# Kernel optimization log

Hardware: AMD Instinct MI355X
Metric: run time of the kernel (lower is better)

## Reference

```python
import jax, jax.numpy as jnp
import numpy as np

B, NIMG, H, W, C = 4, 4, 80, 80, 256
NH = 8
C1 = C // 8          # 32
CPH = C1 // NH       # 4 per-head conv channels
K2D = 4              # deformable attention sampling points
HD2 = C1 // NH       # 4 head dim for 2D deformable attention
INNER = 32           # 3D deformable attention inner dim
DSF = (2, 8, 8)
OSC = jnp.array([2.0, 8.0, 8.0], jnp.float32)


def _bilin2d(img, px, py):
    # img [B,C,H,W]; px,py [B,K] pixel coords -> [B,K,C], zero-padded outside
    Bb, Cc, Hh, Ww = img.shape
    x0 = jnp.floor(px); y0 = jnp.floor(py)
    wx = px - x0; wy = py - y0
    bidx = jnp.arange(Bb)[:, None]
    def g(yy, xx):
        valid = (xx >= 0) & (xx <= Ww - 1) & (yy >= 0) & (yy <= Hh - 1)
        xi = jnp.clip(xx, 0, Ww - 1).astype(jnp.int32)
        yi = jnp.clip(yy, 0, Hh - 1).astype(jnp.int32)
        return img[bidx, :, yi, xi] * valid[..., None]
    return (g(y0, x0) * ((1 - wy) * (1 - wx))[..., None]
          + g(y0, x0 + 1) * ((1 - wy) * wx)[..., None]
          + g(y0 + 1, x0) * (wy * (1 - wx))[..., None]
          + g(y0 + 1, x0 + 1) * (wy * wx)[..., None])


def _trilin(img, z, y, x):
    # img [B,C,D,H,W]; z,y,x [B,K] -> [B,K,C]
    Bb, Cc, Dd, Hh, Ww = img.shape
    z0 = jnp.floor(z); y0 = jnp.floor(y); x0 = jnp.floor(x)
    wz = z - z0; wy = y - y0; wx = x - x0
    bidx = jnp.arange(Bb)[:, None]
    def g(zz, yy, xx):
        valid = (zz >= 0) & (zz <= Dd - 1) & (yy >= 0) & (yy <= Hh - 1) & (xx >= 0) & (xx <= Ww - 1)
        zi = jnp.clip(zz, 0, Dd - 1).astype(jnp.int32)
        yi = jnp.clip(yy, 0, Hh - 1).astype(jnp.int32)
        xi = jnp.clip(xx, 0, Ww - 1).astype(jnp.int32)
        return img[bidx, :, zi, yi, xi] * valid[..., None]
    out = 0.
    for dz in (0., 1.):
        for dy in (0., 1.):
            for dx in (0., 1.):
                w = ((1 - wz) if dz == 0. else wz) * ((1 - wy) if dy == 0. else wy) * ((1 - wx) if dx == 0. else wx)
                out = out + g(z0 + dz, y0 + dy, x0 + dx) * w[..., None]
    return out


def _fwd(x, W_qkv, b_qkv, W_fc, b_fc, W_doff, b_doff, W_dep, b_dep, W_st, b_st,
         W_off2d, b_off2d, W_attw, b_attw, W_val, b_val, W_out2d, b_out2d,
         W_q3, b_q3, W_k3, b_k3, W_v3, b_v3, W_offA, b_offA, W_offB, b_offB,
         W_out3, b_out3, rate1, rate2, nimg):
    xb = jnp.transpose(x, (1, 0, 2))                       # [B, nHW, C]
    Bb = xb.shape[0]
    qkv = xb @ W_qkv + b_qkv                               # [B, nHW, 2*C1]
    # ---------- deformable-conv (ACMix) branch ----------
    f_all = qkv.reshape(Bb, nimg * H * W, 2 * NH, CPH).transpose(0, 2, 1, 3)
    f9 = jnp.einsum('oc,bcnk->bonk', W_fc, f_all) + b_fc[None, :, None, None]
    f_conv = f9.transpose(0, 3, 1, 2).reshape(Bb, 9 * CPH, nimg, H, W)
    fin = f_conv.transpose(0, 2, 1, 3, 4).reshape(Bb * nimg, 9 * CPH, H, W)
    off = jax.lax.conv_general_dilated(fin, W_doff, (1, 1), ((1, 1), (1, 1)),
          dimension_numbers=('NCHW', 'OIHW', 'NCHW')) + b_doff[None, :, None, None]
    off = off.reshape(Bb * nimg, 9, 2, H, W)               # (dy,dx) per 3x3 tap
    hh, ww = jnp.meshgrid(jnp.arange(H, dtype=jnp.float32), jnp.arange(W, dtype=jnp.float32), indexing='ij')
    tap = jnp.arange(9)
    ky = (tap // 3 - 1).astype(jnp.float32); kx = (tap % 3 - 1).astype(jnp.float32)
    py = hh[None, None] + ky[None, :, None, None] + off[:, :, 0]
    px = ww[None, None] + kx[None, :, None, None] + off[:, :, 1]
    samp = _bilin2d(fin, px.reshape(Bb * nimg, -1), py.reshape(Bb * nimg, -1))
    samp = samp.reshape(Bb * nimg, 9, H, W, 9 * CPH).transpose(0, 4, 1, 2, 3)
    sg = samp.reshape(Bb * nimg, CPH, 9, 9, H, W)          # [Bn, g, cin_pg, taps, H, W]
    wg = W_dep.reshape(CPH, 27, 9, 9)                      # [g, out_pg, cin_pg, taps]
    dep = jnp.einsum('bgikhw,goik->bgohw', sg, wg).reshape(Bb * nimg, 27 * CPH, H, W) + b_dep[None, :, None, None]
    oc = dep.reshape(Bb, nimg, 27 * CPH, H, W).transpose(0, 2, 1, 3, 4)
    st_in = oc.reshape(Bb, CPH, 27, nimg, H, W)
    st = jnp.einsum('bginhw,goi->bgonhw', st_in, W_st).reshape(Bb, C, nimg, H, W) + b_st[None, :, None, None, None]
    out_conv = st.transpose(2, 3, 4, 0, 1).reshape(nimg * H * W, Bb, C)
    # ---------- per-frame 2D deformable attention ----------
    qk = qkv.reshape(Bb, nimg, H, W, 2, C1)
    q2 = qk[..., 0, :].reshape(Bb * nimg, H, W, C1)
    k2 = qk[..., 1, :].reshape(Bb * nimg, H, W, C1)
    gy, gx = jnp.meshgrid(jnp.arange(H, dtype=jnp.float32) / (H - 1),
                          jnp.arange(W, dtype=jnp.float32) / (W - 1), indexing='ij')
    ref = jnp.stack([gx, gy], -1)                          # [H,W,2] normalized (x,y)
    off2 = (q2 @ W_off2d + b_off2d).reshape(Bb * nimg, H, W, NH, K2D, 2)
    attw = jax.nn.softmax((q2 @ W_attw + b_attw).reshape(Bb * nimg, H, W, NH, K2D), axis=-1)
    v2 = (k2 @ W_val + b_val).reshape(Bb * nimg, H, W, NH, HD2)
    vimg = v2.transpose(0, 3, 4, 1, 2).reshape(Bb * nimg * NH, HD2, H, W)
    loc = ref[None, :, :, None, None, :] + off2 / jnp.array([W, H], jnp.float32)
    ppx = (loc[..., 0] * (W - 1)).transpose(0, 3, 1, 2, 4).reshape(Bb * nimg * NH, H * W * K2D)
    ppy = (loc[..., 1] * (H - 1)).transpose(0, 3, 1, 2, 4).reshape(Bb * nimg * NH, H * W * K2D)
    s2 = _bilin2d(vimg, ppx, ppy).reshape(Bb * nimg, NH, H, W, K2D, HD2)
    a2 = jnp.einsum('bhwnk,bnhwkd->bhwnd', attw, s2).reshape(Bb * nimg, H, W, C1)
    a2 = (a2 @ W_out2d + b_out2d).reshape(Bb, nimg, H, W, C1)
    # faithful reproduction of the source's frame-concat bug: frames [0,0,1,...,nimg-2]
    idx = jnp.array([0] + list(range(nimg - 1)))
    x3 = a2[:, idx].transpose(0, 4, 1, 2, 3)               # [B, C1, nimg, H, W]
    # ---------- 3D deformable attention ----------
    q3 = jnp.einsum('oc,bcnhw->bonhw', W_q3, x3) + b_q3[None, :, None, None, None]
    hid = jax.lax.conv_general_dilated(q3, W_offA, DSF, ((1, 1), (1, 1), (1, 1)),
          dimension_numbers=('NCDHW', 'OIDHW', 'NCDHW')) + b_offA[None, :, None, None, None]
    hid = jax.nn.gelu(hid)
    off3 = jnp.einsum('oc,bcnhw->bonhw', W_offB, hid) + b_offB[None, :, None, None, None]
    off3 = jnp.tanh(off3) * OSC[None, :, None, None, None]
    npr, hpr, wpr = off3.shape[2], off3.shape[3], off3.shape[4]
    gz, gy2, gx2 = jnp.meshgrid(jnp.arange(npr, dtype=jnp.float32) * 2 + 0.5,
                                jnp.arange(hpr, dtype=jnp.float32) * 8 + 3.5,
                                jnp.arange(wpr, dtype=jnp.float32) * 8 + 3.5, indexing='ij')
    cz = (gz[None] + off3[:, 0]).reshape(Bb, -1)
    cy = (gy2[None] + off3[:, 1]).reshape(Bb, -1)
    cx = (gx2[None] + off3[:, 2]).reshape(Bb, -1)
    kf = jnp.einsum('oc,bcnhw->bonhw', W_k3, x3) + b_k3[None, :, None, None, None]
    vf = jnp.einsum('oc,bcnhw->bonhw', W_v3, x3) + b_v3[None, :, None, None, None]
    ks_ = _trilin(kf, cz, cy, cx)                          # [B, L, INNER]
    vs_ = _trilin(vf, cz, cy, cx)
    qf = q3.reshape(Bb, INNER, -1).transpose(0, 2, 1)      # [B, N, INNER]
    at = jax.nn.softmax(jnp.einsum('bnd,bld->bnl', qf, ks_) * (INNER ** -0.5), axis=-1)
    o3 = jnp.einsum('bnl,bld->bnd', at, vs_).transpose(0, 2, 1).reshape(Bb, INNER, nimg, H, W)
    o3 = jnp.einsum('oc,bcnhw->bonhw', W_out3, o3) + b_out3[None, :, None, None, None]
    xattn = o3.transpose(2, 3, 4, 0, 1).reshape(nimg * H * W, Bb, C)
    return rate1 * xattn + rate2 * out_conv


def _p(key, shape, s=0.02):
    return jax.random.normal(key, shape, jnp.float32) * s


def setup_inputs() -> dict:
    key = jax.random.key(0)
    ks = jax.random.split(key, 20)
    z = lambda *s: jnp.zeros(s, jnp.float32)
    return {
        'x': jax.random.normal(ks[0], (NIMG * H * W, B, C), jnp.float32),
        'W_qkv': _p(ks[1], (C, C // 4)), 'b_qkv': z(C // 4),
        'W_fc': _p(ks[2], (9, 2 * NH)), 'b_fc': z(9),
        'W_doff': _p(ks[3], (18, 9 * CPH, 3, 3), 0.01), 'b_doff': z(18),
        'W_dep': _p(ks[4], (27 * CPH, 9, 3, 3)), 'b_dep': z(27 * CPH),
        'W_st': _p(ks[5], (CPH, C // CPH, 27)), 'b_st': z(C),
        'W_off2d': _p(ks[6], (C1, NH * K2D * 2), 0.01), 'b_off2d': z(NH * K2D * 2),
        'W_attw': _p(ks[7], (C1, NH * K2D)), 'b_attw': z(NH * K2D),
        'W_val': _p(ks[8], (C1, C1)), 'b_val': z(C1),
        'W_out2d': _p(ks[9], (C1, C1)), 'b_out2d': z(C1),
        'W_q3': _p(ks[10], (INNER, C1)), 'b_q3': z(INNER),
        'W_k3': _p(ks[11], (INNER, C1)), 'b_k3': z(INNER),
        'W_v3': _p(ks[12], (INNER, C1)), 'b_v3': z(INNER),
        'W_offA': _p(ks[13], (INNER, INNER, 4, 10, 10), 0.01), 'b_offA': z(INNER),
        'W_offB': _p(ks[14], (3, INNER), 0.01), 'b_offB': z(3),
        'W_out3': _p(ks[15], (C, INNER)), 'b_out3': z(C),
        'rate1': jnp.full((1,), 0.5, jnp.float32),
        'rate2': jnp.full((1,), 0.5, jnp.float32),
        'nimg': NIMG,
    }


def reference(x, W_qkv, b_qkv, W_fc, b_fc, W_doff, b_doff, W_dep, b_dep, W_st, b_st,
              W_off2d, b_off2d, W_attw, b_attw, W_val, b_val, W_out2d, b_out2d,
              W_q3, b_q3, W_k3, b_k3, W_v3, b_v3, W_offA, b_offA, W_offB, b_offB,
              W_out3, b_out3, rate1, rate2, nimg):
    return _fwd(x, W_qkv, b_qkv, W_fc, b_fc, W_doff, b_doff, W_dep, b_dep, W_st, b_st,
                W_off2d, b_off2d, W_attw, b_attw, W_val, b_val, W_out2d, b_out2d,
                W_q3, b_q3, W_k3, b_k3, W_v3, b_v3, W_offA, b_offA, W_offB, b_offB,
                W_out3, b_out3, rate1, rate2, nimg)
```

## Files before the change

### kernel.cpp

```cpp
#include <hip/hip_runtime.h>
#include <math.h>

#define B_     4
#define NIMG_  4
#define H_     80
#define W_     80
#define C_     256
#define NH_    8
#define HW_    6400
#define NQ_    25600
#define NPIX_  102400
#define L3_    200

#define WS_QH   0u
#define WS_KH   3276800u
#define WS_V2   6553600u
#define WS_FING 9830400u
#define WS_OFF  3276800u
#define WS_A2   9830400u
#define WS_Q3   0u
#define WS_KF   3276800u
#define WS_VF   6553600u
#define WS_CRD  9830400u
#define WS_KS   9832800u
#define WS_VS   9858400u
#define WS_O3   3276800u

__global__ __launch_bounds__(256) void k_qkv(const float* __restrict__ x,
        const float* __restrict__ Wq, const float* __restrict__ bq,
        float* __restrict__ qh, float* __restrict__ kh) {
    __shared__ __align__(16) float xs[32][256];
    int t = threadIdx.x;
    int row0 = blockIdx.x * 32;
    for (int it = 0; it < 8; ++it) {
        int idx = t + it * 256;
        int r = idx >> 6;
        int f4 = idx & 63;
        int row = row0 + r;
        int b = row / NQ_, n = row % NQ_;
        const float4* src = (const float4*)(x + ((size_t)n * B_ + b) * C_);
        ((float4*)&xs[r][0])[f4] = src[f4];
    }
    __syncthreads();
    int j = t & 63;
    int rbase = (t >> 6) * 8;
    float acc[8];
    #pragma unroll
    for (int r = 0; r < 8; ++r) acc[r] = 0.f;
    for (int c4 = 0; c4 < 64; ++c4) {
        float w0 = Wq[(c4 * 4 + 0) * 64 + j];
        float w1 = Wq[(c4 * 4 + 1) * 64 + j];
        float w2 = Wq[(c4 * 4 + 2) * 64 + j];
        float w3 = Wq[(c4 * 4 + 3) * 64 + j];
        #pragma unroll
        for (int r = 0; r < 8; ++r) {
            float4 xv = ((const float4*)&xs[rbase + r][0])[c4];
            acc[r] += xv.x * w0 + xv.y * w1 + xv.z * w2 + xv.w * w3;
        }
    }
    float bias = bq[j];
    #pragma unroll
    for (int r = 0; r < 8; ++r) {
        int row = row0 + rbase + r;
        float vres = acc[r] + bias;
        if (j < 32) qh[(size_t)row * 32 + j] = vres;
        else        kh[(size_t)row * 32 + (j - 32)] = vres;
    }
}

__global__ __launch_bounds__(256) void k_fin_v2(const float* __restrict__ qh,
        const float* __restrict__ kh,
        const float* __restrict__ Wfc, const float* __restrict__ bfc,
        const float* __restrict__ Wval, const float* __restrict__ bval,
        float* __restrict__ fing, float* __restrict__ v2) {
    __shared__ float WvalL[1024], WfcL[144], bfcL[9], bvalL[32];
    int t = threadIdx.x;
    for (int d = t; d < 1024; d += 256) WvalL[d] = Wval[d];
    if (t < 144) WfcL[t] = Wfc[t];
    if (t >= 160 && t < 169) bfcL[t - 160] = bfc[t - 160];
    if (t >= 192 && t < 224) bvalL[t - 192] = bval[t - 192];
    __syncthreads();
    int P = blockIdx.x * 256 + t;
    int b = P / NQ_, nq = P % NQ_;
    int n = nq / HW_, hw = nq % HW_;
    int bn = b * NIMG_ + n;
    float q[64];
    const float4* qp = (const float4*)(qh + (size_t)P * 32);
    const float4* kp = (const float4*)(kh + (size_t)P * 32);
    #pragma unroll
    for (int i = 0; i < 8; ++i) ((float4*)q)[i] = qp[i];
    #pragma unroll
    for (int i = 0; i < 8; ++i) ((float4*)q)[8 + i] = kp[i];
    float fo[36];
    #pragma unroll
    for (int k = 0; k < 4; ++k)
        #pragma unroll
        for (int o = 0; o < 9; ++o) fo[k * 9 + o] = bfcL[o];
    for (int c = 0; c < 16; ++c) {
        #pragma unroll
        for (int o = 0; o < 9; ++o) {
            float wv = WfcL[o * 16 + c];
            #pragma unroll
            for (int k = 0; k < 4; ++k) fo[k * 9 + o] += wv * q[c * 4 + k];
        }
    }
    #pragma unroll
    for (int g = 0; g < 4; ++g) {
        float* fp = fing + ((size_t)(g * 16 + bn) * HW_ + hw) * 12;
        ((float4*)fp)[0] = make_float4(fo[g * 9 + 0], fo[g * 9 + 1], fo[g * 9 + 2], fo[g * 9 + 3]);
        ((float4*)fp)[1] = make_float4(fo[g * 9 + 4], fo[g * 9 + 5], fo[g * 9 + 6], fo[g * 9 + 7]);
        ((float4*)fp)[2] = make_float4(fo[g * 9 + 8], 0.f, 0.f, 0.f);
    }
    float vo[32];
    #pragma unroll
    for (int j = 0; j < 32; ++j) vo[j] = bvalL[j];
    for (int c = 0; c < 32; ++c) {
        float qc = q[32 + c];
        #pragma unroll
        for (int j = 0; j < 32; ++j) vo[j] += qc * WvalL[c * 32 + j];
    }
    float* vp = v2 + ((size_t)bn * HW_ + hw) * 32;
    #pragma unroll
    for (int i = 0; i < 8; ++i) ((float4*)vp)[i] = ((float4*)vo)[i];
}

__global__ __launch_bounds__(256) void k_offconv(const float* __restrict__ fing,
        const float* __restrict__ Wdoff, const float* __restrict__ bdoff,
        float* __restrict__ off) {
    __shared__ float Wl[5832];
    int t = threadIdx.x;
    for (int d = t; d < 5832; d += 256) {
        int tap = d / 648, r = d % 648, c = r / 18, o = r % 18;
        Wl[d] = Wdoff[(o * 36 + c) * 9 + tap];
    }
    __syncthreads();
    int P = blockIdx.x * 256 + t;
    int bn = P / HW_, hw = P % HW_;
    int h = hw / W_, w = hw % W_;
    float acc[18];
    #pragma unroll
    for (int o = 0; o < 18; ++o) acc[o] = bdoff[o];
    for (int ky = 0; ky < 3; ++ky) {
        int hh = h + ky - 1;
        if (hh < 0 || hh >= H_) continue;
        for (int kx = 0; kx < 3; ++kx) {
            int ww = w + kx - 1;
            if (ww < 0 || ww >= W_) continue;
            int sp = hh * W_ + ww;
            const float* wl = Wl + (ky * 3 + kx) * 648;
            #pragma unroll
            for (int g = 0; g < 4; ++g) {
                const float4* base = (const float4*)(fing
                        + ((size_t)(g * 16 + bn) * HW_ + sp) * 12);
                float4 p0 = base[0], p1 = base[1], p2 = base[2];
                float vals[9] = {p0.x, p0.y, p0.z, p0.w, p1.x, p1.y, p1.z, p1.w, p2.x};
                #pragma unroll
                for (int idx = 0; idx < 9; ++idx) {
                    const float* w0 = wl + (g * 9 + idx) * 18;
                    float vv = vals[idx];
                    #pragma unroll
                    for (int o = 0; o < 18; ++o) acc[o] += vv * w0[o];
                }
            }
        }
    }
    float* op = off + (size_t)P * 18;
    #pragma unroll
    for (int o = 0; o < 18; ++o) op[o] = acc[o];
}

__global__ __launch_bounds__(256, 6) void k_depst(const float* __restrict__ fing,
        const float* __restrict__ off, const float* __restrict__ Wdep,
        const float* __restrict__ bdep, const float* __restrict__ Wst,
        const float* __restrict__ bst, const float* __restrict__ rate2p,
        float* __restrict__ out) {
    __shared__ __align__(16) float wdepL[2268];
    __shared__ __align__(16) float wstL[1728];
    __shared__ float bdepL[27];
    __shared__ float bstL[64];
    int t = threadIdx.x;
    int bx = blockIdx.x;
    int u = (bx & 7) * 200 + (bx >> 3);
    int chunk = u >> 2, g = u & 3;
    for (int d = t; d < 2268; d += 256) {
        int k = d / 252, r2 = d % 252;
        int i = r2 / 28, o = r2 % 28;
        wdepL[d] = (o < 27) ? Wdep[(size_t)(g * 27 + o) * 81 + i * 9 + k] : 0.f;
    }
    for (int d = t; d < 1728; d += 256) {
        int i = d >> 6, o = d & 63;
        wstL[d] = Wst[g * 1728 + o * 27 + i];
    }
    if (t < 27) bdepL[t] = bdep[g * 27 + t];
    if (t >= 32 && t < 96) bstL[t - 32] = bst[g * 64 + (t - 32)];
    __syncthreads();
    int P = chunk * 256 + t;
    int bn = P / HW_, hw = P % HW_;
    int h = hw / W_, w = hw % W_;
    int b = bn >> 2, n = bn & 3;
    const float* finb = fing + (size_t)(g * 16 + bn) * (HW_ * 12);
    const float* offp = off + (size_t)P * 18;
    float acc[27];
    #pragma unroll
    for (int o = 0; o < 27; ++o) acc[o] = 0.f;
    float hf = (float)h, wf = (float)w;
    #pragma unroll 1
    for (int k = 0; k < 9; ++k) {
        float2 od = *(const float2*)(offp + k * 2);
        float py = hf + (float)(k / 3 - 1) + od.x;
        float px = wf + (float)(k % 3 - 1) + od.y;
        float y0f = floorf(py), x0f = floorf(px);
        float wy = py - y0f, wx = px - x0f;
        float wy0 = 1.f - wy, wx0 = 1.f - wx;
        float vy0 = (y0f >= 0.f && y0f <= 79.f) ? 1.f : 0.f;
        float vy1 = (y0f >= -1.f && y0f <= 78.f) ? 1.f : 0.f;
        float vx0 = (x0f >= 0.f && x0f <= 79.f) ? 1.f : 0.f;
        float vx1 = (x0f >= -1.f && x0f <= 78.f) ? 1.f : 0.f;
        int yi0 = (int)fminf(fmaxf(y0f, 0.f), 79.f);
        int yi1 = (int)fminf(fmaxf(y0f + 1.f, 0.f), 79.f);
        int xi0 = (int)fminf(fmaxf(x0f, 0.f), 79.f);
        int xi1 = (int)fminf(fmaxf(x0f + 1.f, 0.f), 79.f);
        float w00 = wy0 * wx0 * vy0 * vx0;
        float w01 = wy0 * wx  * vy0 * vx1;
        float w10 = wy  * wx0 * vy1 * vx0;
        float w11 = wy  * wx  * vy1 * vx1;
        const float4* c00 = (const float4*)(finb + (size_t)(yi0 * W_ + xi0) * 12);
        const float4* c01 = (const float4*)(finb + (size_t)(yi0 * W_ + xi1) * 12);
        const float4* c10 = (const float4*)(finb + (size_t)(yi1 * W_ + xi0) * 12);
        const float4* c11 = (const float4*)(finb + (size_t)(yi1 * W_ + xi1) * 12);
        float s[9];
        {
            float4 p0 = c00[0], p1 = c00[1], p2 = c00[2];
            s[0] = w00 * p0.x; s[1] = w00 * p0.y; s[2] = w00 * p0.z; s[3] = w00 * p0.w;
            s[4] = w00 * p1.x; s[5] = w00 * p1.y; s[6] = w00 * p1.z; s[7] = w00 * p1.w;
            s[8] = w00 * p2.x;
        }
        {
            float4 p0 = c01[0], p1 = c01[1], p2 = c01[2];
            s[0] += w01 * p0.x; s[1] += w01 * p0.y; s[2] += w01 * p0.z; s[3] += w01 * p0.w;
            s[4] += w01 * p1.x; s[5] += w01 * p1.y; s[6] += w01 * p1.z; s[7] += w01 * p1.w;
            s[8] += w01 * p2.x;
        }
        {
            float4 p0 = c10[0], p1 = c10[1], p2 = c10[2];
            s[0] += w10 * p0.x; s[1] += w10 * p0.y; s[2] += w10 * p0.z; s[3] += w10 * p0.w;
            s[4] += w10 * p1.x; s[5] += w10 * p1.y; s[6] += w10 * p1.z; s[7] += w10 * p1.w;
            s[8] += w10 * p2.x;
        }
        {
            float4 p0 = c11[0], p1 = c11[1], p2 = c11[2];
            s[0] += w11 * p0.x; s[1] += w11 * p0.y; s[2] += w11 * p0.z; s[3] += w11 * p0.w;
            s[4] += w11 * p1.x; s[5] += w11 * p1.y; s[6] += w11 * p1.z; s[7] += w11 * p1.w;
            s[8] += w11 * p2.x;
        }
        const float* wk = wdepL + k * 252;
        #pragma unroll
        for (int i = 0; i < 9; ++i) {
            float si = s[i];
            const float4* rw = (const float4*)(wk + i * 28);
            float4 q0 = rw[0], q1 = rw[1], q2 = rw[2], q3v = rw[3];
            float4 q4 = rw[4], q5 = rw[5], q6 = rw[6];
            acc[0]  += si * q0.x;  acc[1]  += si * q0.y;  acc[2]  += si * q0.z;  acc[3]  += si * q0.w;
            acc[4]  += si * q1.x;  acc[5]  += si * q1.y;  acc[6]  += si * q1.z;  acc[7]  += si * q1.w;
            acc[8]  += si * q2.x;  acc[9]  += si * q2.y;  acc[10] += si * q2.z;  acc[11] += si * q2.w;
            acc[12] += si * q3v.x; acc[13] += si * q3v.y; acc[14] += si * q3v.z; acc[15] += si * q3v.w;
            acc[16] += si * q4.x;  acc[17] += si * q4.y;  acc[18] += si * q4.z;  acc[19] += si * q4.w;
            acc[20] += si * q5.x;  acc[21] += si * q5.y;  acc[22] += si * q5.z;  acc[23] += si * q5.w;
            acc[24] += si * q6.x;  acc[25] += si * q6.y;  acc[26] += si * q6.z;
        }
    }
    #pragma unroll
    for (int i = 0; i < 27; ++i) acc[i] += bdepL[i];
    float r2v = rate2p[0];
    float* ob = out + ((size_t)(n * HW_ + hw) * B_ + b) * C_ + g * 64;
    #pragma unroll 1
    for (int half = 0; half < 2; ++half) {
        float ro[32];
        #pragma unroll
        for (int o = 0; o < 32; ++o) ro[o] = bstL[half * 32 + o];
        #pragma unroll
        for (int i = 0; i < 27; ++i) {
            float ai = acc[i];
            const float4* rw = (const float4*)(wstL + i * 64 + half * 32);
            #pragma unroll
            for (int j = 0; j < 8; ++j) {
                float4 wv = rw[j];
                ro[j * 4 + 0] += ai * wv.x;
                ro[j * 4 + 1] += ai * wv.y;
                ro[j * 4 + 2] += ai * wv.z;
                ro[j * 4 + 3] += ai * wv.w;
            }
        }
        float4* obv = (float4*)(ob + half * 32);
        #pragma unroll
        for (int o4 = 0; o4 < 8; ++o4)
            obv[o4] = make_float4(r2v * ro[o4 * 4 + 0], r2v * ro[o4 * 4 + 1],
                                  r2v * ro[o4 * 4 + 2], r2v * ro[o4 * 4 + 3]);
    }
}

__global__ __launch_bounds__(256) void k_attn2d(const float* __restrict__ qh,
        const float* __restrict__ v2,
        const float* __restrict__ Woff, const float* __restrict__ boff,
        const float* __restrict__ Watt, const float* __restrict__ batt,
        const float* __restrict__ Wout, const float* __restrict__ bout,
        float* __restrict__ a2) {
    __shared__ float WoffL[2048], WattL[1024], WoutL[1024];
    __shared__ float boffL[64], battL[32], boutL[32];
    int t = threadIdx.x;
    for (int d = t; d < 2048; d += 256) WoffL[d] = Woff[d];
    for (int d = t; d < 1024; d += 256) { WattL[d] = Watt[d]; WoutL[d] = Wout[d]; }
    if (t < 64) boffL[t] = boff[t];
    else if (t < 96) battL[t - 64] = batt[t - 64];
    else if (t < 128) boutL[t - 96] = bout[t - 96];
    __syncthreads();
    int P = blockIdx.x * 256 + t;
    int b = P / NQ_, nq = P % NQ_;
    int n = nq / HW_, hw = nq % HW_;
    int h = hw / W_, w = hw % W_;
    int bn = b * NIMG_ + n;
    float q[32];
    const float4* qp = (const float4*)(qh + (size_t)P * 32);
    #pragma unroll
    for (int i = 0; i < 8; ++i) ((float4*)q)[i] = qp[i];
    const float* vbase = v2 + (size_t)bn * HW_ * 32;
    float a2v[32];
    #pragma unroll
    for (int i = 0; i < 32; ++i) a2v[i] = 0.f;
    for (int nh = 0; nh < 8; ++nh) {
        float t0 = battL[nh * 4 + 0], t1 = battL[nh * 4 + 1];
        float t2 = battL[nh * 4 + 2], t3 = battL[nh * 4 + 3];
        for (int c = 0; c < 32; ++c) {
            float qc = q[c];
            const float* wr = WattL + c * 32 + nh * 4;
            t0 += qc * wr[0]; t1 += qc * wr[1]; t2 += qc * wr[2]; t3 += qc * wr[3];
        }
        float m = fmaxf(fmaxf(t0, t1), fmaxf(t2, t3));
        float e0 = expf(t0 - m), e1 = expf(t1 - m), e2 = expf(t2 - m), e3 = expf(t3 - m);
        float inv = 1.f / (e0 + e1 + e2 + e3);
        float pk[4] = {e0 * inv, e1 * inv, e2 * inv, e3 * inv};
        #pragma unroll
        for (int kk = 0; kk < 4; ++kk) {
            int j0 = nh * 8 + kk * 2;
            float ox = boffL[j0], oy = boffL[j0 + 1];
            for (int c = 0; c < 32; ++c) {
                float qc = q[c];
                ox += qc * WoffL[c * 64 + j0];
                oy += qc * WoffL[c * 64 + j0 + 1];
            }
            float ppx = (float)w + ox * (79.f / 80.f);
            float ppy = (float)h + oy * (79.f / 80.f);
            float x0 = floorf(ppx), y0 = floorf(ppy);
            float wx = ppx - x0, wy = ppy - y0;
            float s0 = 0.f, s1 = 0.f, s2 = 0.f, s3 = 0.f;
            #pragma unroll
            for (int cy = 0; cy < 2; ++cy) {
                float yf = y0 + (float)cy;
                if (yf < 0.f || yf > 79.f) continue;
                float wyf = cy ? wy : 1.f - wy;
                int yi = (int)yf;
                #pragma unroll
                for (int cx = 0; cx < 2; ++cx) {
                    float xf = x0 + (float)cx;
                    if (xf < 0.f || xf > 79.f) continue;
                    float wgt = wyf * (cx ? wx : 1.f - wx);
                    int xi = (int)xf;
                    float4 vv = *(const float4*)(vbase + ((size_t)yi * W_ + xi) * 32 + nh * 4);
                    s0 += wgt * vv.x; s1 += wgt * vv.y; s2 += wgt * vv.z; s3 += wgt * vv.w;
                }
            }
            float p = pk[kk];
            a2v[nh * 4 + 0] += p * s0; a2v[nh * 4 + 1] += p * s1;
            a2v[nh * 4 + 2] += p * s2; a2v[nh * 4 + 3] += p * s3;
        }
    }
    float ro[32];
    #pragma unroll
    for (int o = 0; o < 32; ++o) ro[o] = boutL[o];
    for (int c = 0; c < 32; ++c) {
        float ac = a2v[c];
        const float* wr = WoutL + c * 32;
        #pragma unroll
        for (int o = 0; o < 32; ++o) ro[o] += ac * wr[o];
    }
    float* op = a2 + ((size_t)bn * HW_ + hw) * 32;
    #pragma unroll
    for (int i = 0; i < 8; ++i) ((float4*)op)[i] = ((float4*)ro)[i];
}

__global__ __launch_bounds__(256) void k_qkv3(const float* __restrict__ a2,
        const float* __restrict__ Wq3, const float* __restrict__ bq3,
        const float* __restrict__ Wk3, const float* __restrict__ bk3,
        const float* __restrict__ Wv3, const float* __restrict__ bv3,
        float* __restrict__ q3, float* __restrict__ kf, float* __restrict__ vf) {
    __shared__ float Wq3L[1024], Wk3L[1024], Wv3L[1024];
    __shared__ float bq3L[32], bk3L[32], bv3L[32];
    int t = threadIdx.x;
    for (int d = t; d < 1024; d += 256) {
        Wq3L[d] = Wq3[d]; Wk3L[d] = Wk3[d]; Wv3L[d] = Wv3[d];
    }
    if (t < 32) { bq3L[t] = bq3[t]; bk3L[t] = bk3[t]; bv3L[t] = bv3[t]; }
    __syncthreads();
    int idx = blockIdx.x * 256 + t;
    int bn = idx / HW_, hw = idx % HW_;
    int b = bn >> 2, n = bn & 3;
    int ns = (n == 0) ? 0 : n - 1;
    const float* src = a2 + ((size_t)(b * 4 + ns) * HW_ + hw) * 32;
    float v[32];
    #pragma unroll
    for (int i = 0; i < 8; ++i) ((float4*)v)[i] = ((const float4*)src)[i];
    float oq[32], ok[32], ov[32];
    #pragma unroll
    for (int o = 0; o < 32; ++o) {
        float aq = bq3L[o], ak = bk3L[o], av = bv3L[o];
        #pragma unroll
        for (int c = 0; c < 32; ++c) {
            aq += Wq3L[o * 32 + c] * v[c];
            ak += Wk3L[o * 32 + c] * v[c];
            av += Wv3L[o * 32 + c] * v[c];
        }
        oq[o] = aq; ok[o] = ak; ov[o] = av;
    }
    float* qo = q3 + (size_t)idx * 32;
    float* ko = kf + (size_t)idx * 32;
    float* vo = vf + (size_t)idx * 32;
    #pragma unroll
    for (int i = 0; i < 8; ++i) {
        ((float4*)qo)[i] = ((float4*)oq)[i];
        ((float4*)ko)[i] = ((float4*)ok)[i];
        ((float4*)vo)[i] = ((float4*)ov)[i];
    }
}

__global__ __launch_bounds__(256) void k_offs3d(const float* __restrict__ q3,
        const float* __restrict__ WoffA, const float* __restrict__ boffA,
        const float* __restrict__ WoffB, const float* __restrict__ boffB,
        float* __restrict__ coords) {
    __shared__ float red[4][128];
    __shared__ float hidl[128];
    int t = threadIdx.x;
    int blk = blockIdx.x;
    int zo = blk / 100, r = blk % 100, ho = r / 10, wo = r % 10;
    float acc[4][32];
    #pragma unroll
    for (int b = 0; b < 4; ++b)
        #pragma unroll
        for (int o = 0; o < 32; ++o) acc[b][o] = 0.f;
    for (int tap = t; tap < 400; tap += 256) {
        int kz = tap / 100, r2 = tap % 100, ky = r2 / 10, kx = r2 % 10;
        int zi = zo * 2 + kz - 1, hi = ho * 8 + ky - 1, wi = wo * 8 + kx - 1;
        if (zi < 0 || zi >= NIMG_ || hi < 0 || hi >= H_ || wi < 0 || wi >= W_) continue;
        const float* wb = WoffA + tap;
        int sp = hi * W_ + wi;
        for (int c = 0; c < 32; ++c) {
            float vb[4];
            #pragma unroll
            for (int b = 0; b < 4; ++b)
                vb[b] = q3[((size_t)(b * 4 + zi) * HW_ + sp) * 32 + c];
            #pragma unroll
            for (int o = 0; o < 32; ++o) {
                float wv = wb[(o * 32 + c) * 400];
                #pragma unroll
                for (int b = 0; b < 4; ++b) acc[b][o] += vb[b] * wv;
            }
        }
    }
    #pragma unroll
    for (int b = 0; b < 4; ++b)
        #pragma unroll
        for (int o = 0; o < 32; ++o)
            for (int sh = 32; sh >= 1; sh >>= 1)
                acc[b][o] += __shfl_xor(acc[b][o], sh);
    int lane = t & 63, wv = t >> 6;
    if (lane == 0)
        for (int b = 0; b < 4; ++b)
            for (int o = 0; o < 32; ++o) red[wv][b * 32 + o] = acc[b][o];
    __syncthreads();
    if (t < 128) {
        float v = red[0][t] + red[1][t] + red[2][t] + red[3][t] + boffA[t & 31];
        float v3 = v * v * v;
        hidl[t] = 0.5f * v * (1.f + tanhf(0.7978845608028654f * (v + 0.044715f * v3)));
    }
    __syncthreads();
    if (t < 12) {
        int b = t / 3, j = t % 3;
        float a = boffB[j];
        for (int o = 0; o < 32; ++o) a += WoffB[j * 32 + o] * hidl[b * 32 + o];
        float osc = (j == 0) ? 2.f : 8.f;
        float base = (j == 0) ? (zo * 2 + 0.5f) : ((j == 1) ? (ho * 8 + 3.5f) : (wo * 8 + 3.5f));
        coords[((size_t)b * L3_ + blk) * 3 + j] = base + tanhf(a) * osc;
    }
}

__global__ __launch_bounds__(256) void k_trisample(const float* __restrict__ kf,
        const float* __restrict__ vf, const float* __restrict__ coords,
        float* __restrict__ ks, float* __restrict__ vs) {
    int t = threadIdx.x;
    int wv = blockIdx.x * 4 + (t >> 6);
    int b = wv / L3_, l = wv % L3_;
    int lane = t & 63;
    int c = lane & 31;
    const float* src = (lane < 32) ? kf : vf;
    float* dst = (lane < 32) ? ks : vs;
    const float* cp = coords + ((size_t)b * L3_ + l) * 3;
    float cz = cp[0], cy = cp[1], cx = cp[2];
    float z0 = floorf(cz), y0 = floorf(cy), x0 = floorf(cx);
    float wz = cz - z0, wy = cy - y0, wx = cx - x0;
    float acc = 0.f;
    #pragma unroll
    for (int dz = 0; dz < 2; ++dz) {
        float zf = z0 + (float)dz;
        if (zf < 0.f || zf > 3.f) continue;
        float wzf = dz ? wz : 1.f - wz;
        int zi = (int)zf;
        #pragma unroll
        for (int dy = 0; dy < 2; ++dy) {
            float yf = y0 + (float)dy;
            if (yf < 0.f || yf > 79.f) continue;
            float wyf = wzf * (dy ? wy : 1.f - wy);
            int yi = (int)yf;
            #pragma unroll
            for (int dx = 0; dx < 2; ++dx) {
                float xf = x0 + (float)dx;
                if (xf < 0.f || xf > 79.f) continue;
                float wgt = wyf * (dx ? wx : 1.f - wx);
                int xi = (int)xf;
                acc += wgt * src[((size_t)(b * 4 + zi) * HW_ + yi * W_ + xi) * 32 + c];
            }
        }
    }
    dst[((size_t)b * L3_ + l) * 32 + c] = acc;
}

__global__ __launch_bounds__(256) void k_attn3d(const float* __restrict__ q3,
        const float* __restrict__ ks, const float* __restrict__ vs,
        float* __restrict__ o3) {
    __shared__ __align__(16) float ksl[L3_ * 32];
    __shared__ __align__(16) float vsl[L3_ * 32];
    int t = threadIdx.x;
    int b = blockIdx.x / 100;
    int chunk = blockIdx.x % 100;
    const float4* ksg = (const float4*)(ks + (size_t)b * L3_ * 32);
    const float4* vsg = (const float4*)(vs + (size_t)b * L3_ * 32);
    for (int d = t; d < L3_ * 8; d += 256) {
        ((float4*)ksl)[d] = ksg[d];
        ((float4*)vsl)[d] = vsg[d];
    }
    __syncthreads();
    int N = chunk * 256 + t;
    float q[32];
    const float4* qp = (const float4*)(q3 + ((size_t)b * NQ_ + N) * 32);
    #pragma unroll
    for (int i = 0; i < 8; ++i) ((float4*)q)[i] = qp[i];
    const float scale = 0.17677669529663687f;
    float den = 0.f;
    float o[32];
    #pragma unroll
    for (int c = 0; c < 32; ++c) o[c] = 0.f;
    for (int l = 0; l < L3_; ++l) {
        const float4* kp = (const float4*)(ksl + l * 32);
        float s = 0.f;
        #pragma unroll
        for (int c4 = 0; c4 < 8; ++c4) {
            float4 kv = kp[c4];
            s += q[c4 * 4 + 0] * kv.x + q[c4 * 4 + 1] * kv.y + q[c4 * 4 + 2] * kv.z + q[c4 * 4 + 3] * kv.w;
        }
        float p = expf(s * scale);
        den += p;
        const float4* vp = (const float4*)(vsl + l * 32);
        #pragma unroll
        for (int c4 = 0; c4 < 8; ++c4) {
            float4 vv = vp[c4];
            o[c4 * 4 + 0] += p * vv.x; o[c4 * 4 + 1] += p * vv.y;
            o[c4 * 4 + 2] += p * vv.z; o[c4 * 4 + 3] += p * vv.w;
        }
    }
    float inv = 1.f / den;
    float* op = o3 + ((size_t)b * NQ_ + N) * 32;
    #pragma unroll
    for (int c = 0; c < 32; ++c) op[c] = o[c] * inv;
}

__global__ __launch_bounds__(256) void k_final(const float* __restrict__ o3,
        const float* __restrict__ W, const float* __restrict__ bias,
        const float* __restrict__ r1p, float* __restrict__ out) {
    __shared__ float o3T[32 * 128];
    __shared__ float WT[32 * 260];
    int t = threadIdx.x;
    int R0 = blockIdx.x * 128;
    {
        int row = t >> 1, k0 = (t & 1) * 16;
        int R = R0 + row;
        int b = R & 3, N = R >> 2;
        const float* src = o3 + ((size_t)b * NQ_ + N) * 32 + k0;
        #pragma unroll
        for (int j = 0; j < 16; ++j) o3T[(k0 + j) * 128 + row] = src[j];
    }
    for (int d = t; d < 8192; d += 256) {
        int c = d >> 5, k = d & 31;
        WT[k * 260 + c] = W[d];
    }
    __syncthreads();
    int tc = t & 15;
    int tr = t >> 4;
    int r0 = tr * 8;
    float acc[8][16];
    #pragma unroll
    for (int i = 0; i < 8; ++i)
        #pragma unroll
        for (int j = 0; j < 16; ++j) acc[i][j] = 0.f;
    #pragma unroll 1
    for (int k = 0; k < 32; ++k) {
        float a[8];
        *(float4*)&a[0] = *(const float4*)&o3T[k * 128 + r0];
        *(float4*)&a[4] = *(const float4*)&o3T[k * 128 + r0 + 4];
        float wv[16];
        #pragma unroll
        for (int ci = 0; ci < 16; ++ci) wv[ci] = WT[k * 260 + tc + 16 * ci];
        #pragma unroll
        for (int i = 0; i < 8; ++i)
            #pragma unroll
            for (int j = 0; j < 16; ++j) acc[i][j] += a[i] * wv[j];
    }
    float r1 = r1p[0];
    float bs[16];
    #pragma unroll
    for (int ci = 0; ci < 16; ++ci) bs[ci] = bias[tc + 16 * ci];
    #pragma unroll 1
    for (int i = 0; i < 8; ++i) {
        size_t rowbase = (size_t)(R0 + r0 + i) * 256;
        #pragma unroll
        for (int j = 0; j < 16; ++j) {
            size_t oi = rowbase + tc + 16 * j;
            out[oi] = r1 * (acc[i][j] + bs[j]) + out[oi];
        }
    }
}

extern "C" void kernel_launch(void* const* d_in, const int* in_sizes, int n_in,
                              void* d_out, int out_size, void* d_ws, size_t ws_size,
                              hipStream_t stream) {
    (void)in_sizes; (void)n_in; (void)out_size; (void)ws_size;
    const float* x      = (const float*)d_in[0];
    const float* W_qkv  = (const float*)d_in[1];
    const float* b_qkv  = (const float*)d_in[2];
    const float* W_fc   = (const float*)d_in[3];
    const float* b_fc   = (const float*)d_in[4];
    const float* W_doff = (const float*)d_in[5];
    const float* b_doff = (const float*)d_in[6];
    const float* W_dep  = (const float*)d_in[7];
    const float* b_dep  = (const float*)d_in[8];
    const float* W_st   = (const float*)d_in[9];
    const float* b_st   = (const float*)d_in[10];
    const float* W_off2d= (const float*)d_in[11];
    const float* b_off2d= (const float*)d_in[12];
    const float* W_attw = (const float*)d_in[13];
    const float* b_attw = (const float*)d_in[14];
    const float* W_val  = (const float*)d_in[15];
    const float* b_val  = (const float*)d_in[16];
    const float* W_out2d= (const float*)d_in[17];
    const float* b_out2d= (const float*)d_in[18];
    const float* W_q3   = (const float*)d_in[19];
    const float* b_q3   = (const float*)d_in[20];
    const float* W_k3   = (const float*)d_in[21];
    const float* b_k3   = (const float*)d_in[22];
    const float* W_v3   = (const float*)d_in[23];
    const float* b_v3   = (const float*)d_in[24];
    const float* W_offA = (const float*)d_in[25];
    const float* b_offA = (const float*)d_in[26];
    const float* W_offB = (const float*)d_in[27];
    const float* b_offB = (const float*)d_in[28];
    const float* W_out3 = (const float*)d_in[29];
    const float* b_out3 = (const float*)d_in[30];
    const float* rate1  = (const float*)d_in[31];
    const float* rate2  = (const float*)d_in[32];

    float* ws  = (float*)d_ws;
    float* out = (float*)d_out;
    float* qhp = ws + WS_QH;
    float* khp = ws + WS_KH;
    float* fng = ws + WS_FING;
    float* off = ws + WS_OFF;
    float* v2  = ws + WS_V2;
    float* a2  = ws + WS_A2;
    float* q3  = ws + WS_Q3;
    float* kf  = ws + WS_KF;
    float* vf  = ws + WS_VF;
    float* crd = ws + WS_CRD;
    float* ks  = ws + WS_KS;
    float* vs  = ws + WS_VS;
    float* o3w = ws + WS_O3;

    k_qkv      <<<3200,   256, 0, stream>>>(x, W_qkv, b_qkv, qhp, khp);
    k_fin_v2   <<<400,    256, 0, stream>>>(qhp, khp, W_fc, b_fc, W_val, b_val, fng, v2);
    k_offconv  <<<400,    256, 0, stream>>>(fng, W_doff, b_doff, off);
    k_depst    <<<1600,   256, 0, stream>>>(fng, off, W_dep, b_dep, W_st, b_st, rate2, out);
    k_attn2d   <<<400,    256, 0, stream>>>(qhp, v2, W_off2d, b_off2d, W_attw, b_attw, W_out2d, b_out2d, a2);
    k_qkv3     <<<400,    256, 0, stream>>>(a2, W_q3, b_q3, W_k3, b_k3, W_v3, b_v3, q3, kf, vf);
    k_offs3d   <<<200,    256, 0, stream>>>(q3, W_offA, b_offA, W_offB, b_offB, crd);
    k_trisample<<<200,    256, 0, stream>>>(kf, vf, crd, ks, vs);
    k_attn3d   <<<400,    256, 0, stream>>>(q3, ks, vs, o3w);
    k_final    <<<800,    256, 0, stream>>>(o3w, W_out3, b_out3, rate1, out);
}
```

Baseline: 1.053 ms.

## Interleave per-group fin features per pixel and preload deformable offsets

The fin feature buffer changes from a group-major layout to a pixel-major layout with all four groups' 12 floats contiguous (48 floats per pixel). The offset conv can then read one contiguous 192-byte span per neighbour instead of four scattered ones. The deformable-conv kernel hoists its nine offset loads into registers ahead of the sampling loop, and its occupancy hint drops from 6 to 4 blocks per CU. The trade-off is that each depst block, which handles one group, now gathers with a 192-byte stride and uses only 48 of every 192 bytes, which may waste cache lines in that sampling-heavy kernel.

```diff
diff --git a/kernel.cpp b/kernel.cpp
--- a/kernel.cpp
+++ b/kernel.cpp
@@ -15,7 +15,7 @@
 #define WS_QH   0u
 #define WS_KH   3276800u
 #define WS_V2   6553600u
-#define WS_FING 9830400u
+#define WS_FIN2 9830400u
 #define WS_OFF  3276800u
 #define WS_A2   9830400u
 #define WS_Q3   0u
@@ -72,7 +72,7 @@
         const float* __restrict__ kh,
         const float* __restrict__ Wfc, const float* __restrict__ bfc,
         const float* __restrict__ Wval, const float* __restrict__ bval,
-        float* __restrict__ fing, float* __restrict__ v2) {
+        float* __restrict__ fin2, float* __restrict__ v2) {
     __shared__ float WvalL[1024], WfcL[144], bfcL[9], bvalL[32];
     int t = threadIdx.x;
     for (int d = t; d < 1024; d += 256) WvalL[d] = Wval[d];
@@ -104,12 +104,12 @@
             for (int k = 0; k < 4; ++k) fo[k * 9 + o] += wv * q[c * 4 + k];
         }
     }
+    float* fp = fin2 + ((size_t)bn * HW_ + hw) * 48;
     #pragma unroll
     for (int g = 0; g < 4; ++g) {
-        float* fp = fing + ((size_t)(g * 16 + bn) * HW_ + hw) * 12;
-        ((float4*)fp)[0] = make_float4(fo[g * 9 + 0], fo[g * 9 + 1], fo[g * 9 + 2], fo[g * 9 + 3]);
-        ((float4*)fp)[1] = make_float4(fo[g * 9 + 4], fo[g * 9 + 5], fo[g * 9 + 6], fo[g * 9 + 7]);
-        ((float4*)fp)[2] = make_float4(fo[g * 9 + 8], 0.f, 0.f, 0.f);
+        ((float4*)fp)[g * 3 + 0] = make_float4(fo[g * 9 + 0], fo[g * 9 + 1], fo[g * 9 + 2], fo[g * 9 + 3]);
+        ((float4*)fp)[g * 3 + 1] = make_float4(fo[g * 9 + 4], fo[g * 9 + 5], fo[g * 9 + 6], fo[g * 9 + 7]);
+        ((float4*)fp)[g * 3 + 2] = make_float4(fo[g * 9 + 8], 0.f, 0.f, 0.f);
     }
     float vo[32];
     #pragma unroll
@@ -124,7 +124,7 @@
     for (int i = 0; i < 8; ++i) ((float4*)vp)[i] = ((float4*)vo)[i];
 }
 
-__global__ __launch_bounds__(256) void k_offconv(const float* __restrict__ fing,
+__global__ __launch_bounds__(256) void k_offconv(const float* __restrict__ fin2,
         const float* __restrict__ Wdoff, const float* __restrict__ bdoff,
         float* __restrict__ off) {
     __shared__ float Wl[5832];
@@ -147,12 +147,11 @@
             int ww = w + kx - 1;
             if (ww < 0 || ww >= W_) continue;
             int sp = hh * W_ + ww;
+            const float4* base = (const float4*)(fin2 + ((size_t)bn * HW_ + sp) * 48);
             const float* wl = Wl + (ky * 3 + kx) * 648;
             #pragma unroll
             for (int g = 0; g < 4; ++g) {
-                const float4* base = (const float4*)(fing
-                        + ((size_t)(g * 16 + bn) * HW_ + sp) * 12);
-                float4 p0 = base[0], p1 = base[1], p2 = base[2];
+                float4 p0 = base[g * 3 + 0], p1 = base[g * 3 + 1], p2 = base[g * 3 + 2];
                 float vals[9] = {p0.x, p0.y, p0.z, p0.w, p1.x, p1.y, p1.z, p1.w, p2.x};
                 #pragma unroll
                 for (int idx = 0; idx < 9; ++idx) {
@@ -169,7 +168,7 @@
     for (int o = 0; o < 18; ++o) op[o] = acc[o];
 }
 
-__global__ __launch_bounds__(256, 6) void k_depst(const float* __restrict__ fing,
+__global__ __launch_bounds__(256, 4) void k_depst(const float* __restrict__ fin2,
         const float* __restrict__ off, const float* __restrict__ Wdep,
         const float* __restrict__ bdep, const float* __restrict__ Wst,
         const float* __restrict__ bst, const float* __restrict__ rate2p,
@@ -198,17 +197,21 @@
     int bn = P / HW_, hw = P % HW_;
     int h = hw / W_, w = hw % W_;
     int b = bn >> 2, n = bn & 3;
-    const float* finb = fing + (size_t)(g * 16 + bn) * (HW_ * 12);
-    const float* offp = off + (size_t)P * 18;
+    const float* finb = fin2 + (size_t)bn * (HW_ * 48) + g * 12;
+    float2 offs[9];
+    {
+        const float2* op2 = (const float2*)(off + (size_t)P * 18);
+        #pragma unroll
+        for (int k = 0; k < 9; ++k) offs[k] = op2[k];
+    }
     float acc[27];
     #pragma unroll
     for (int o = 0; o < 27; ++o) acc[o] = 0.f;
     float hf = (float)h, wf = (float)w;
     #pragma unroll 1
     for (int k = 0; k < 9; ++k) {
-        float2 od = *(const float2*)(offp + k * 2);
-        float py = hf + (float)(k / 3 - 1) + od.x;
-        float px = wf + (float)(k % 3 - 1) + od.y;
+        float py = hf + (float)(k / 3 - 1) + offs[k].x;
+        float px = wf + (float)(k % 3 - 1) + offs[k].y;
         float y0f = floorf(py), x0f = floorf(px);
         float wy = py - y0f, wx = px - x0f;
         float wy0 = 1.f - wy, wx0 = 1.f - wx;
@@ -224,10 +227,10 @@
         float w01 = wy0 * wx  * vy0 * vx1;
         float w10 = wy  * wx0 * vy1 * vx0;
         float w11 = wy  * wx  * vy1 * vx1;
-        const float4* c00 = (const float4*)(finb + (size_t)(yi0 * W_ + xi0) * 12);
-        const float4* c01 = (const float4*)(finb + (size_t)(yi0 * W_ + xi1) * 12);
-        const float4* c10 = (const float4*)(finb + (size_t)(yi1 * W_ + xi0) * 12);
-        const float4* c11 = (const float4*)(finb + (size_t)(yi1 * W_ + xi1) * 12);
+        const float4* c00 = (const float4*)(finb + (size_t)(yi0 * W_ + xi0) * 48);
+        const float4* c01 = (const float4*)(finb + (size_t)(yi0 * W_ + xi1) * 48);
+        const float4* c10 = (const float4*)(finb + (size_t)(yi1 * W_ + xi0) * 48);
+        const float4* c11 = (const float4*)(finb + (size_t)(yi1 * W_ + xi1) * 48);
         float s[9];
         {
             float4 p0 = c00[0], p1 = c00[1], p2 = c00[2];
@@ -679,7 +682,7 @@
     float* out = (float*)d_out;
     float* qhp = ws + WS_QH;
     float* khp = ws + WS_KH;
-    float* fng = ws + WS_FING;
+    float* fn2 = ws + WS_FIN2;
     float* off = ws + WS_OFF;
     float* v2  = ws + WS_V2;
     float* a2  = ws + WS_A2;
@@ -692,9 +695,9 @@
     float* o3w = ws + WS_O3;
 
     k_qkv      <<<3200,   256, 0, stream>>>(x, W_qkv, b_qkv, qhp, khp);
-    k_fin_v2   <<<400,    256, 0, stream>>>(qhp, khp, W_fc, b_fc, W_val, b_val, fng, v2);
-    k_offconv  <<<400,    256, 0, stream>>>(fng, W_doff, b_doff, off);
-    k_depst    <<<1600,   256, 0, stream>>>(fng, off, W_dep, b_dep, W_st, b_st, rate2, out);
+    k_fin_v2   <<<400,    256, 0, stream>>>(qhp, khp, W_fc, b_fc, W_val, b_val, fn2, v2);
+    k_offconv  <<<400,    256, 0, stream>>>(fn2, W_doff, b_doff, off);
+    k_depst    <<<1600,   256, 0, stream>>>(fn2, off, W_dep, b_dep, W_st, b_st, rate2, out);
     k_attn2d   <<<400,    256, 0, stream>>>(qhp, v2, W_off2d, b_off2d, W_attw, b_attw, W_out2d, b_out2d, a2);
     k_qkv3     <<<400,    256, 0, stream>>>(a2, W_q3, b_q3, W_k3, b_k3, W_v3, b_v3, q3, kf, vf);
     k_offs3d   <<<200,    256, 0, stream>>>(q3, W_offA, b_offA, W_offB, b_offB, crd);
```

New measurement: 886.5 us. 1.19x faster.
